# Optimization experiments

Measured on AMD Instinct MI355X. Metric: run time of the kernel, lower is better.

## Reference

```python
import jax, jax.numpy as jnp
import numpy as np

N_NODES = 25000
N_EDGES = 50000
NODE_DIM = 64
EDGE_DIM = 16
HIDDEN_DIM = 128


def setup_inputs() -> dict:
    key = jax.random.key(0)
    ks = jax.random.split(key, 12)
    s = 0.05  # small init scale for params
    return {
        "x": jax.random.normal(ks[0], (N_NODES, NODE_DIM), dtype=jnp.float32),
        "edge_index": jax.random.randint(ks[1], (2, N_EDGES), 0, N_NODES, dtype=jnp.int64),
        "edge_attr": jax.random.normal(ks[2], (N_EDGES, EDGE_DIM), dtype=jnp.float32),
        "W1": jax.random.normal(ks[3], (HIDDEN_DIM, EDGE_DIM), dtype=jnp.float32) * s,
        "b1": jax.random.normal(ks[4], (HIDDEN_DIM,), dtype=jnp.float32) * s,
        "W2": jax.random.normal(ks[5], (NODE_DIM * NODE_DIM, HIDDEN_DIM), dtype=jnp.float32) * s,
        "b2": jax.random.normal(ks[6], (NODE_DIM * NODE_DIM,), dtype=jnp.float32) * s,
        "w_ih": jax.random.normal(ks[7], (3 * NODE_DIM, NODE_DIM), dtype=jnp.float32) * s,
        "w_hh": jax.random.normal(ks[8], (3 * NODE_DIM, NODE_DIM), dtype=jnp.float32) * s,
        "b_ih": jax.random.normal(ks[9], (3 * NODE_DIM,), dtype=jnp.float32) * s,
        "b_hh": jax.random.normal(ks[10], (3 * NODE_DIM,), dtype=jnp.float32) * s,
    }


def reference(x, edge_index, edge_attr, W1, b1, W2, b2, w_ih, w_hh, b_ih, b_hh):
    n_nodes, d = x.shape
    src, dst = edge_index[0], edge_index[1]
    # edge-conditioned weight matrices: MLP_edge(e_ij) -> (E, d, d)
    h = jax.nn.gelu(edge_attr @ W1.T + b1, approximate=False)
    edge_w = (h @ W2.T + b2).reshape(-1, d, d)
    # per-edge message: W_e @ x_src  (gather + batched matvec)
    messages = jnp.einsum('eij,ej->ei', edge_w, x[src])
    # scatter-add into destination nodes
    agg = jax.ops.segment_sum(messages, dst, num_segments=n_nodes)
    # GRUCell(agg, x): input=agg, hidden=x  (PyTorch gate layout r,z,n)
    gi = agg @ w_ih.T + b_ih
    gh = x @ w_hh.T + b_hh
    i_r, i_z, i_n = jnp.split(gi, 3, axis=-1)
    h_r, h_z, h_n = jnp.split(gh, 3, axis=-1)
    r = jax.nn.sigmoid(i_r + h_r)
    z = jax.nn.sigmoid(i_z + h_z)
    n = jnp.tanh(i_n + r * h_n)
    return (1.0 - z) * n + z * x
```

## Files before the change

kernel.cpp:

```cpp
#include <hip/hip_runtime.h>
#include <math.h>


constexpr int N_NODES  = 25000;
constexpr int N_EDGES  = 50000;
constexpr int NODE_DIM = 64;
constexpr int EDGE_DIM = 16;
constexpr int HID      = 128;
constexpr int FS       = 65;

typedef __attribute__((ext_vector_type(8))) _Float16 half8;
typedef __attribute__((ext_vector_type(4))) float    f32x4;

constexpr int G_MS  = 128;
constexpr int G_PK  = 270;

__global__ __launch_bounds__(256) void prep_kernel(
    const float* __restrict__ W2, const float* __restrict__ b2,
    const float* __restrict__ w_ih, const float* __restrict__ w_hh,
    _Float16* __restrict__ Wpk, _Float16* __restrict__ b2pk,
    _Float16* __restrict__ gpk, float* __restrict__ agg)
{
    int b = blockIdx.x;
    if (b < G_MS) {
        float4* a4 = (float4*)agg;
        const float4 z = make_float4(0.f, 0.f, 0.f, 0.f);
        for (int i = b * 256 + threadIdx.x; i < N_NODES * NODE_DIM / 4; i += G_MS * 256)
            a4[i] = z;
        return;
    }
    int c = (b - G_MS) * 256 + threadIdx.x;
    if (c < 65536) {
        int lane = c & 63, mt = (c >> 6) & 3, ks = (c >> 8) & 3, j = c >> 10;
        int i   = mt * 16 + (lane & 15);
        int col = ks * 32 + ((lane >> 4) & 3) * 8;
        const float* src = W2 + (size_t)(i * 64 + j) * HID + col;
        half8 o;
#pragma unroll
        for (int q = 0; q < 8; ++q) o[q] = (_Float16)src[q];
        ((half8*)Wpk)[c] = o;
    } else if (c < 65536 + 512) {
        int c2 = c - 65536;
        int lane = c2 & 63, mt = (c2 >> 6) & 3, ks2 = (c2 >> 8) & 1;
        int i = mt * 16 + (lane & 15);
        int j = ks2 * 32 + ((lane >> 4) & 3) * 8;
        const float* src = b2 + i * 64 + j;
        half8 o;
#pragma unroll
        for (int q = 0; q < 8; ++q) o[q] = (_Float16)src[q];
        ((half8*)b2pk)[c2] = o;
    } else if (c < 65536 + 512 + 3072) {
        int c3 = c - (65536 + 512);
        int lane = c3 & 63, ks = (c3 >> 6) & 1;
        int t2 = c3 >> 7;
        int nt = t2 % 12, mat = t2 / 12;
        int g = nt * 16 + (lane & 15);
        int k = ks * 32 + ((lane >> 4) & 3) * 8;
        const float* src = (mat == 0 ? w_ih : w_hh) + (size_t)g * 64 + k;
        half8 o;
#pragma unroll
        for (int q = 0; q < 8; ++q) o[q] = (_Float16)src[q];
        ((half8*)gpk)[c3] = o;
    }
}

__global__ __launch_bounds__(256, 3) void edge_msg_mfma_kernel(
    const float*    __restrict__ edge_attr,
    const float*    __restrict__ W1,
    const float*    __restrict__ b1,
    const float*    __restrict__ x,
    const int*      __restrict__ edge_index,
    const _Float16* __restrict__ Wpk,
    const _Float16* __restrict__ b2pk,
    float* __restrict__ agg)
{
    __shared__ float xsh[64 * 68];
    __shared__ float msgred[64 * 67];
    __shared__ float W1s[128 * 16];
    __shared__ float b1s[128];
    __shared__ int   dsts[64];
    half8* hshf = (half8*)msgred;

    const int e0   = blockIdx.x * 64;
    const int t    = threadIdx.x;
    const int mt   = t >> 6;
    const int lane = t & 63;

    {
        int le = t >> 2, sub = t & 3;
        int e = e0 + le;
        int s = -1;
        if (e < N_EDGES) {
            if (sub == 0) dsts[le] = edge_index[N_EDGES + e];
            s = edge_index[e];
        } else if (sub == 0) {
            dsts[le] = -1;
        }
#pragma unroll
        for (int q = 0; q < 4; ++q) {
            float4 v = make_float4(0.f, 0.f, 0.f, 0.f);
            if ((unsigned)s < (unsigned)N_NODES)
                v = ((const float4*)x)[(size_t)s * 16 + sub * 4 + q];
            *(float4*)&xsh[le * 68 + sub * 16 + q * 4] = v;
        }
    }

#pragma unroll
    for (int r = 0; r < 8; ++r) W1s[t + r * 256] = W1[t + r * 256];
    if (t < 128) b1s[t] = b1[t];
    __syncthreads();

    {
        const int ks = mt;
        int e = e0 + lane;
        float ea[16];
        if (e < N_EDGES) {
            const float4* ea4 = (const float4*)(edge_attr + (size_t)e * EDGE_DIM);
#pragma unroll
            for (int q = 0; q < 4; ++q) {
                float4 v = ea4[q];
                ea[q * 4] = v.x; ea[q * 4 + 1] = v.y; ea[q * 4 + 2] = v.z; ea[q * 4 + 3] = v.w;
            }
        } else {
#pragma unroll
            for (int d = 0; d < 16; ++d) ea[d] = 0.f;
        }
        const int fbase = ((lane >> 4) * 4 + ks) * FS + (lane & 15);
#pragma unroll
        for (int kc = 0; kc < 4; ++kc) {
            half8 hh;
#pragma unroll
            for (int kk = 0; kk < 8; ++kk) {
                int k = ks * 32 + kc * 8 + kk;
                float acc = b1s[k];
                const float* w = &W1s[k * 16];
#pragma unroll
                for (int d = 0; d < EDGE_DIM; ++d) acc += ea[d] * w[d];
                float g = 0.5f * acc * (1.0f + erff(acc * 0.70710678118654752f));
                hh[kk] = (_Float16)g;
            }
            hshf[fbase + kc * 16] = hh;
        }
    }
    __syncthreads();

    half8 hf[4][4];
#pragma unroll
    for (int nt = 0; nt < 4; ++nt)
#pragma unroll
        for (int ks = 0; ks < 4; ++ks)
            hf[nt][ks] = hshf[(nt * 4 + ks) * FS + lane];
    __syncthreads();

    const f32x4 zero4 = {0.f, 0.f, 0.f, 0.f};
    f32x4 msg[4];
#pragma unroll
    for (int nt = 0; nt < 4; ++nt) msg[nt] = zero4;

    const half8* wpk8 = (const half8*)Wpk;
    const int mbase = mt * 64 + lane;

    half8 aA[4], aB[4];
#pragma unroll
    for (int ks = 0; ks < 4; ++ks) aA[ks] = wpk8[(size_t)mbase + ks * 256];

#pragma unroll 1
    for (int j = 0; j < 64; j += 2) {
        {
            size_t nb = (size_t)(j + 1) * 1024 + mbase;
#pragma unroll
            for (int ks = 0; ks < 4; ++ks) aB[ks] = wpk8[nb + ks * 256];
        }
        {
            float gv[4];
#pragma unroll
            for (int nt = 0; nt < 4; ++nt) gv[nt] = xsh[(nt * 16 + (lane & 15)) * 68 + j];
            f32x4 P[4];
#pragma unroll
            for (int ks = 0; ks < 4; ++ks)
#pragma unroll
                for (int nt = 0; nt < 4; ++nt)
                    P[nt] = __builtin_amdgcn_mfma_f32_16x16x32_f16(
                        aA[ks], hf[nt][ks], ks == 0 ? zero4 : P[nt], 0, 0, 0);
#pragma unroll
            for (int nt = 0; nt < 4; ++nt)
#pragma unroll
                for (int r = 0; r < 4; ++r) msg[nt][r] += gv[nt] * P[nt][r];
        }
        if (j + 2 < 64) {
            size_t nb = (size_t)(j + 2) * 1024 + mbase;
#pragma unroll
            for (int ks = 0; ks < 4; ++ks) aA[ks] = wpk8[nb + ks * 256];
        }
        {
            float gv[4];
#pragma unroll
            for (int nt = 0; nt < 4; ++nt) gv[nt] = xsh[(nt * 16 + (lane & 15)) * 68 + j + 1];
            f32x4 P[4];
#pragma unroll
            for (int ks = 0; ks < 4; ++ks)
#pragma unroll
                for (int nt = 0; nt < 4; ++nt)
                    P[nt] = __builtin_amdgcn_mfma_f32_16x16x32_f16(
                        aB[ks], hf[nt][ks], ks == 0 ? zero4 : P[nt], 0, 0, 0);
#pragma unroll
            for (int nt = 0; nt < 4; ++nt)
#pragma unroll
                for (int r = 0; r < 4; ++r) msg[nt][r] += gv[nt] * P[nt][r];
        }
    }

#pragma unroll
    for (int ks2 = 0; ks2 < 2; ++ks2) {
        half8 gf[4];
#pragma unroll
        for (int nt = 0; nt < 4; ++nt) {
            const float* gp = &xsh[(nt * 16 + (lane & 15)) * 68 + ks2 * 32 + ((lane >> 4) & 3) * 8];
            float4 lo = *(const float4*)gp;
            float4 hi = *(const float4*)(gp + 4);
            half8 g8;
            g8[0] = (_Float16)lo.x; g8[1] = (_Float16)lo.y;
            g8[2] = (_Float16)lo.z; g8[3] = (_Float16)lo.w;
            g8[4] = (_Float16)hi.x; g8[5] = (_Float16)hi.y;
            g8[6] = (_Float16)hi.z; g8[7] = (_Float16)hi.w;
            gf[nt] = g8;
        }
        half8 bf8 = ((const half8*)b2pk)[ks2 * 256 + mt * 64 + lane];
#pragma unroll
        for (int nt = 0; nt < 4; ++nt)
            msg[nt] = __builtin_amdgcn_mfma_f32_16x16x32_f16(bf8, gf[nt], msg[nt], 0, 0, 0);
    }

#pragma unroll
    for (int nt = 0; nt < 4; ++nt)
#pragma unroll
        for (int r = 0; r < 4; ++r) {
            int i = mt * 16 + ((lane >> 4) & 3) * 4 + r;
            int e = nt * 16 + (lane & 15);
            msgred[i * 67 + e] = msg[nt][r];
        }
    __syncthreads();

#pragma unroll 1
    for (int ee = mt; ee < 64; ee += 4) {
        int d = dsts[ee];
        if (e0 + ee < N_EDGES && (unsigned)d < (unsigned)N_NODES)
            atomicAdd(agg + (size_t)d * NODE_DIM + lane, msgred[lane * 67 + ee]);
    }
}

__global__ __launch_bounds__(256) void gru_mfma_kernel(
    const float* __restrict__ agg,
    const float* __restrict__ x,
    const _Float16* __restrict__ gpk,
    const float* __restrict__ b_ih,
    const float* __restrict__ b_hh,
    float* __restrict__ out)
{
    const int t = threadIdx.x, wave = t >> 6, lane = t & 63;
    const int n0 = blockIdx.x * 64;

    int arow = n0 + wave * 16 + (lane & 15);
    if (arow >= N_NODES) arow = N_NODES - 1;
    const int kcol = ((lane >> 4) & 3) * 8;
    half8 aF[2], xF[2];
#pragma unroll
    for (int ks = 0; ks < 2; ++ks) {
        const float* ap = agg + (size_t)arow * 64 + ks * 32 + kcol;
        const float* xp = x   + (size_t)arow * 64 + ks * 32 + kcol;
        float4 a0 = *(const float4*)ap, a1 = *(const float4*)(ap + 4);
        float4 x0 = *(const float4*)xp, x1 = *(const float4*)(xp + 4);
        half8 af, xf;
        af[0] = (_Float16)a0.x; af[1] = (_Float16)a0.y; af[2] = (_Float16)a0.z; af[3] = (_Float16)a0.w;
        af[4] = (_Float16)a1.x; af[5] = (_Float16)a1.y; af[6] = (_Float16)a1.z; af[7] = (_Float16)a1.w;
        xf[0] = (_Float16)x0.x; xf[1] = (_Float16)x0.y; xf[2] = (_Float16)x0.z; xf[3] = (_Float16)x0.w;
        xf[4] = (_Float16)x1.x; xf[5] = (_Float16)x1.y; xf[6] = (_Float16)x1.z; xf[7] = (_Float16)x1.w;
        aF[ks] = af; xF[ks] = xf;
    }

    const half8* g8 = (const half8*)gpk;
    const f32x4 zero4 = {0.f, 0.f, 0.f, 0.f};
    f32x4 accI[12], accH[12];
#pragma unroll
    for (int nt = 0; nt < 12; ++nt) {
        half8 b0 = g8[((0 * 12 + nt) * 2 + 0) * 64 + lane];
        half8 b1f = g8[((0 * 12 + nt) * 2 + 1) * 64 + lane];
        f32x4 a = __builtin_amdgcn_mfma_f32_16x16x32_f16(aF[0], b0, zero4, 0, 0, 0);
        accI[nt] = __builtin_amdgcn_mfma_f32_16x16x32_f16(aF[1], b1f, a, 0, 0, 0);
        half8 c0 = g8[((1 * 12 + nt) * 2 + 0) * 64 + lane];
        half8 c1 = g8[((1 * 12 + nt) * 2 + 1) * 64 + lane];
        f32x4 h0 = __builtin_amdgcn_mfma_f32_16x16x32_f16(xF[0], c0, zero4, 0, 0, 0);
        accH[nt] = __builtin_amdgcn_mfma_f32_16x16x32_f16(xF[1], c1, h0, 0, 0, 0);
    }

    const int nodeBase = n0 + wave * 16 + ((lane >> 4) & 3) * 4;
    const int dlo = lane & 15;
#pragma unroll
    for (int q = 0; q < 4; ++q) {
        int d = q * 16 + dlo;
        float bi0 = b_ih[d], bi1 = b_ih[64 + d], bi2 = b_ih[128 + d];
        float bh0 = b_hh[d], bh1 = b_hh[64 + d], bh2 = b_hh[128 + d];
#pragma unroll
        for (int r = 0; r < 4; ++r) {
            int node = nodeBase + r;
            if (node < N_NODES) {
                float I0 = accI[q][r] + bi0, I1 = accI[q + 4][r] + bi1, I2 = accI[q + 8][r] + bi2;
                float H0 = accH[q][r] + bh0, H1 = accH[q + 4][r] + bh1, H2 = accH[q + 8][r] + bh2;
                float rg = 1.f / (1.f + expf(-(I0 + H0)));
                float z  = 1.f / (1.f + expf(-(I1 + H1)));
                float nn = tanhf(I2 + rg * H2);
                float xv = x[(size_t)node * 64 + d];
                out[(size_t)node * 64 + d] = (1.f - z) * nn + z * xv;
            }
        }
    }
}

extern "C" void kernel_launch(void* const* d_in, const int* in_sizes, int n_in,
                              void* d_out, int out_size, void* d_ws, size_t ws_size,
                              hipStream_t stream)
{
    const float* x          = (const float*)d_in[0];
    const int*   edge_index = (const int*)  d_in[1];
    const float* edge_attr  = (const float*)d_in[2];
    const float* W1         = (const float*)d_in[3];
    const float* b1         = (const float*)d_in[4];
    const float* W2         = (const float*)d_in[5];
    const float* b2         = (const float*)d_in[6];
    const float* w_ih       = (const float*)d_in[7];
    const float* w_hh       = (const float*)d_in[8];
    const float* b_ih       = (const float*)d_in[9];
    const float* b_hh       = (const float*)d_in[10];
    float* out = (float*)d_out;

    char* ws = (char*)d_ws;
    ws += (size_t)N_EDGES * HID * sizeof(_Float16);
    _Float16* Wpk  = (_Float16*)ws;
    ws += (size_t)65536 * 8 * sizeof(_Float16);
    _Float16* b2pk = (_Float16*)ws;
    ws += (size_t)512 * 8 * sizeof(_Float16);
    _Float16* gpk  = (_Float16*)ws;
    ws += (size_t)64 * 192 * sizeof(float);
    ws += (size_t)64 * 192 * sizeof(float);
    float* agg = (float*)ws;

    prep_kernel<<<dim3(G_MS + G_PK), dim3(256), 0, stream>>>(
        W2, b2, w_ih, w_hh, Wpk, b2pk, gpk, agg);

    edge_msg_mfma_kernel<<<dim3((N_EDGES + 63) / 64), dim3(256), 0, stream>>>(
        edge_attr, W1, b1, x, edge_index, Wpk, b2pk, agg);

    gru_mfma_kernel<<<dim3((N_NODES + 63) / 64), dim3(256), 0, stream>>>(
        agg, x, gpk, b_ih, b_hh, out);
}
```

Before: 94.28 us.

## Process 128 edges per block to reuse each W2 fragment across twice the edges

Doubles the edge tile per block from 64 to 128. Each streamed W2 (Wpk) fragment now feeds twice as many MFMAs, which halves global W2 traffic per edge. Shared buffers, the hidden-fragment registers and the message accumulators grow to match. Launch bounds drop from 3 to 2 blocks per CU, and there are half as many blocks, so occupancy and register pressure are the risk.

```diff
diff --git a/kernel.cpp b/kernel.cpp
--- a/kernel.cpp
+++ b/kernel.cpp
@@ -8,6 +8,8 @@
 constexpr int EDGE_DIM = 16;
 constexpr int HID      = 128;
 constexpr int FS       = 65;
+constexpr int BE       = 128;
+constexpr int MP       = 131;
 
 typedef __attribute__((ext_vector_type(8))) _Float16 half8;
 typedef __attribute__((ext_vector_type(4))) float    f32x4;
@@ -64,7 +66,7 @@
     }
 }
 
-__global__ __launch_bounds__(256, 3) void edge_msg_mfma_kernel(
+__global__ __launch_bounds__(256, 2) void edge_msg_mfma_kernel(
     const float*    __restrict__ edge_attr,
     const float*    __restrict__ W1,
     const float*    __restrict__ b1,
@@ -74,35 +76,31 @@
     const _Float16* __restrict__ b2pk,
     float* __restrict__ agg)
 {
-    __shared__ float xsh[64 * 68];
-    __shared__ float msgred[64 * 67];
+    __shared__ float xsh[BE * 68];
+    __shared__ float msgred[64 * MP];
     __shared__ float W1s[128 * 16];
     __shared__ float b1s[128];
-    __shared__ int   dsts[64];
+    __shared__ int   dsts[BE];
     half8* hshf = (half8*)msgred;
 
-    const int e0   = blockIdx.x * 64;
+    const int e0   = blockIdx.x * BE;
     const int t    = threadIdx.x;
     const int mt   = t >> 6;
     const int lane = t & 63;
 
-    {
-        int le = t >> 2, sub = t & 3;
+    if (t < BE) dsts[t] = (e0 + t < N_EDGES) ? edge_index[N_EDGES + e0 + t] : -1;
+#pragma unroll
+    for (int r = 0; r < 8; ++r) {
+        int idx = t + r * 256;
+        int le = idx >> 4, q = idx & 15;
         int e = e0 + le;
-        int s = -1;
+        float4 v = make_float4(0.f, 0.f, 0.f, 0.f);
         if (e < N_EDGES) {
-            if (sub == 0) dsts[le] = edge_index[N_EDGES + e];
-            s = edge_index[e];
-        } else if (sub == 0) {
-            dsts[le] = -1;
-        }
-#pragma unroll
-        for (int q = 0; q < 4; ++q) {
-            float4 v = make_float4(0.f, 0.f, 0.f, 0.f);
+            int s = edge_index[e];
             if ((unsigned)s < (unsigned)N_NODES)
-                v = ((const float4*)x)[(size_t)s * 16 + sub * 4 + q];
-            *(float4*)&xsh[le * 68 + sub * 16 + q * 4] = v;
-        }
+                v = ((const float4*)x)[(size_t)s * 16 + q];
+        }
+        *(float4*)&xsh[le * 68 + q * 4] = v;
     }
 
 #pragma unroll
@@ -112,50 +110,54 @@
 
     {
         const int ks = mt;
-        int e = e0 + lane;
-        float ea[16];
-        if (e < N_EDGES) {
-            const float4* ea4 = (const float4*)(edge_attr + (size_t)e * EDGE_DIM);
-#pragma unroll
-            for (int q = 0; q < 4; ++q) {
-                float4 v = ea4[q];
-                ea[q * 4] = v.x; ea[q * 4 + 1] = v.y; ea[q * 4 + 2] = v.z; ea[q * 4 + 3] = v.w;
+#pragma unroll
+        for (int p = 0; p < 2; ++p) {
+            int el = p * 64 + lane;
+            int e = e0 + el;
+            float ea[16];
+            if (e < N_EDGES) {
+                const float4* ea4 = (const float4*)(edge_attr + (size_t)e * EDGE_DIM);
+#pragma unroll
+                for (int q = 0; q < 4; ++q) {
+                    float4 v = ea4[q];
+                    ea[q * 4] = v.x; ea[q * 4 + 1] = v.y; ea[q * 4 + 2] = v.z; ea[q * 4 + 3] = v.w;
+                }
+            } else {
+#pragma unroll
+                for (int d = 0; d < 16; ++d) ea[d] = 0.f;
             }
-        } else {
-#pragma unroll
-            for (int d = 0; d < 16; ++d) ea[d] = 0.f;
-        }
-        const int fbase = ((lane >> 4) * 4 + ks) * FS + (lane & 15);
-#pragma unroll
-        for (int kc = 0; kc < 4; ++kc) {
-            half8 hh;
-#pragma unroll
-            for (int kk = 0; kk < 8; ++kk) {
-                int k = ks * 32 + kc * 8 + kk;
-                float acc = b1s[k];
-                const float* w = &W1s[k * 16];
-#pragma unroll
-                for (int d = 0; d < EDGE_DIM; ++d) acc += ea[d] * w[d];
-                float g = 0.5f * acc * (1.0f + erff(acc * 0.70710678118654752f));
-                hh[kk] = (_Float16)g;
+            const int fbase = ((el >> 4) * 4 + ks) * FS + (el & 15);
+#pragma unroll
+            for (int kc = 0; kc < 4; ++kc) {
+                half8 hh;
+#pragma unroll
+                for (int kk = 0; kk < 8; ++kk) {
+                    int k = ks * 32 + kc * 8 + kk;
+                    float acc = b1s[k];
+                    const float* w = &W1s[k * 16];
+#pragma unroll
+                    for (int d = 0; d < EDGE_DIM; ++d) acc += ea[d] * w[d];
+                    float g = 0.5f * acc * (1.0f + erff(acc * 0.70710678118654752f));
+                    hh[kk] = (_Float16)g;
+                }
+                hshf[fbase + kc * 16] = hh;
             }
-            hshf[fbase + kc * 16] = hh;
         }
     }
     __syncthreads();
 
-    half8 hf[4][4];
-#pragma unroll
-    for (int nt = 0; nt < 4; ++nt)
+    half8 hf[8][4];
+#pragma unroll
+    for (int nt = 0; nt < 8; ++nt)
 #pragma unroll
         for (int ks = 0; ks < 4; ++ks)
             hf[nt][ks] = hshf[(nt * 4 + ks) * FS + lane];
     __syncthreads();
 
     const f32x4 zero4 = {0.f, 0.f, 0.f, 0.f};
-    f32x4 msg[4];
-#pragma unroll
-    for (int nt = 0; nt < 4; ++nt) msg[nt] = zero4;
+    f32x4 msg[8];
+#pragma unroll
+    for (int nt = 0; nt < 8; ++nt) msg[nt] = zero4;
 
     const half8* wpk8 = (const half8*)Wpk;
     const int mbase = mt * 64 + lane;
@@ -172,9 +174,9 @@
             for (int ks = 0; ks < 4; ++ks) aB[ks] = wpk8[nb + ks * 256];
         }
         {
-            float gv[4];
-#pragma unroll
-            for (int nt = 0; nt < 4; ++nt) gv[nt] = xsh[(nt * 16 + (lane & 15)) * 68 + j];
+            float gv[8];
+#pragma unroll
+            for (int nt = 0; nt < 8; ++nt) gv[nt] = xsh[(nt * 16 + (lane & 15)) * 68 + j];
             f32x4 P[4];
 #pragma unroll
             for (int ks = 0; ks < 4; ++ks)
@@ -186,6 +188,16 @@
             for (int nt = 0; nt < 4; ++nt)
 #pragma unroll
                 for (int r = 0; r < 4; ++r) msg[nt][r] += gv[nt] * P[nt][r];
+#pragma unroll
+            for (int ks = 0; ks < 4; ++ks)
+#pragma unroll
+                for (int nt = 4; nt < 8; ++nt)
+                    P[nt - 4] = __builtin_amdgcn_mfma_f32_16x16x32_f16(
+                        aA[ks], hf[nt][ks], ks == 0 ? zero4 : P[nt - 4], 0, 0, 0);
+#pragma unroll
+            for (int nt = 4; nt < 8; ++nt)
+#pragma unroll
+                for (int r = 0; r < 4; ++r) msg[nt][r] += gv[nt] * P[nt - 4][r];
         }
         if (j + 2 < 64) {
             size_t nb = (size_t)(j + 2) * 1024 + mbase;
@@ -193,9 +205,9 @@
             for (int ks = 0; ks < 4; ++ks) aA[ks] = wpk8[nb + ks * 256];
         }
         {
-            float gv[4];
-#pragma unroll
-            for (int nt = 0; nt < 4; ++nt) gv[nt] = xsh[(nt * 16 + (lane & 15)) * 68 + j + 1];
+            float gv[8];
+#pragma unroll
+            for (int nt = 0; nt < 8; ++nt) gv[nt] = xsh[(nt * 16 + (lane & 15)) * 68 + j + 1];
             f32x4 P[4];
 #pragma unroll
             for (int ks = 0; ks < 4; ++ks)
@@ -207,14 +219,24 @@
             for (int nt = 0; nt < 4; ++nt)
 #pragma unroll
                 for (int r = 0; r < 4; ++r) msg[nt][r] += gv[nt] * P[nt][r];
+#pragma unroll
+            for (int ks = 0; ks < 4; ++ks)
+#pragma unroll
+                for (int nt = 4; nt < 8; ++nt)
+                    P[nt - 4] = __builtin_amdgcn_mfma_f32_16x16x32_f16(
+                        aB[ks], hf[nt][ks], ks == 0 ? zero4 : P[nt - 4], 0, 0, 0);
+#pragma unroll
+            for (int nt = 4; nt < 8; ++nt)
+#pragma unroll
+                for (int r = 0; r < 4; ++r) msg[nt][r] += gv[nt] * P[nt - 4][r];
         }
     }
 
 #pragma unroll
     for (int ks2 = 0; ks2 < 2; ++ks2) {
-        half8 gf[4];
-#pragma unroll
-        for (int nt = 0; nt < 4; ++nt) {
+        half8 bf8 = ((const half8*)b2pk)[ks2 * 256 + mt * 64 + lane];
+#pragma unroll
+        for (int nt = 0; nt < 8; ++nt) {
             const float* gp = &xsh[(nt * 16 + (lane & 15)) * 68 + ks2 * 32 + ((lane >> 4) & 3) * 8];
             float4 lo = *(const float4*)gp;
             float4 hi = *(const float4*)(gp + 4);
@@ -223,29 +245,25 @@
             g8[2] = (_Float16)lo.z; g8[3] = (_Float16)lo.w;
             g8[4] = (_Float16)hi.x; g8[5] = (_Float16)hi.y;
             g8[6] = (_Float16)hi.z; g8[7] = (_Float16)hi.w;
-            gf[nt] = g8;
-        }
-        half8 bf8 = ((const half8*)b2pk)[ks2 * 256 + mt * 64 + lane];
-#pragma unroll
-        for (int nt = 0; nt < 4; ++nt)
-            msg[nt] = __builtin_amdgcn_mfma_f32_16x16x32_f16(bf8, gf[nt], msg[nt], 0, 0, 0);
-    }
-
-#pragma unroll
-    for (int nt = 0; nt < 4; ++nt)
+            msg[nt] = __builtin_amdgcn_mfma_f32_16x16x32_f16(bf8, g8, msg[nt], 0, 0, 0);
+        }
+    }
+
+#pragma unroll
+    for (int nt = 0; nt < 8; ++nt)
 #pragma unroll
         for (int r = 0; r < 4; ++r) {
             int i = mt * 16 + ((lane >> 4) & 3) * 4 + r;
             int e = nt * 16 + (lane & 15);
-            msgred[i * 67 + e] = msg[nt][r];
+            msgred[i * MP + e] = msg[nt][r];
         }
     __syncthreads();
 
 #pragma unroll 1
-    for (int ee = mt; ee < 64; ee += 4) {
+    for (int ee = mt; ee < BE; ee += 4) {
         int d = dsts[ee];
         if (e0 + ee < N_EDGES && (unsigned)d < (unsigned)N_NODES)
-            atomicAdd(agg + (size_t)d * NODE_DIM + lane, msgred[lane * 67 + ee]);
+            atomicAdd(agg + (size_t)d * NODE_DIM + lane, msgred[lane * MP + ee]);
     }
 }
 
@@ -347,7 +365,7 @@
     prep_kernel<<<dim3(G_MS + G_PK), dim3(256), 0, stream>>>(
         W2, b2, w_ih, w_hh, Wpk, b2pk, gpk, agg);
 
-    edge_msg_mfma_kernel<<<dim3((N_EDGES + 63) / 64), dim3(256), 0, stream>>>(
+    edge_msg_mfma_kernel<<<dim3((N_EDGES + BE - 1) / BE), dim3(256), 0, stream>>>(
         edge_attr, W1, b1, x, edge_index, Wpk, b2pk, agg);
 
     gru_mfma_kernel<<<dim3((N_NODES + 63) / 64), dim3(256), 0, stream>>>(
```

After: 134.3 us. +42.4%, slower.
